# Performance work log

Measured on AMD Instinct MI355X. Metric: run time of the kernel, lower is better.

## Reference

```python
import jax, jax.numpy as jnp
import numpy as np

B, N, P, T = 128, 64, 128, 168


def setup_inputs() -> dict:
    key = jax.random.key(0)
    k1, k2, k3, k4, k5 = jax.random.split(key, 5)
    x = jax.random.normal(k1, (B, N, P), dtype=jnp.float32)
    x_i = jax.random.randint(k2, (B, P), 0, T)
    g = jax.random.normal(k3, (N * N, N * N), dtype=jnp.float32)
    weights = jax.random.normal(k4, (N * N, 1), dtype=jnp.float32)
    alphas = jax.random.uniform(k5, (1, T), dtype=jnp.float32)
    return {"x": x, "x_i": x_i, "g": g, "weights": weights, "alphas": alphas}


def reference(x, x_i, g, weights, alphas):
    # x: [b, N, p], x_i: [b, p] int in [0, T), g: [N*N, N*N]
    n = x.shape[1]
    F = (g @ (weights ** 2)) @ alphas          # [N*N, T]
    wg = F.T.reshape(-1, n, n)                 # [T, N, N]
    f_ = wg[x_i]                               # [b, p, N, N] (gather)
    xt = jnp.swapaxes(x, 1, 2)                 # [b, p, N]
    # matmul(f_, x_[...,None]) then sum over (p, last) == einsum then sum over p
    Z = jnp.einsum('bpij,bpj->bi', f_, xt)     # [b, N]
    return (Z, F)
```

## Files before the change

### kernel.cpp

```cpp
#include <hip/hip_runtime.h>
#include <hip/hip_bf16.h>


#define GN 4096
#define TT 168
#define BB 128
#define NN 64
#define PP 128

__global__ __launch_bounds__(256) void k_rowdot(
    const float* __restrict__ g, const float* __restrict__ w,
    const float* __restrict__ alphas, float* __restrict__ v,
    float* __restrict__ Fout) {
  const int row = blockIdx.x;
  const int t = threadIdx.x;
  const float4* g4 = (const float4*)(g + (size_t)row * GN);
  const float4* w4 = (const float4*)w;
  float s = 0.f;
#pragma unroll
  for (int it = 0; it < 4; ++it) {
    int idx = t + it * 256;
    float4 a = g4[idx];
    float4 b = w4[idx];
    s += a.x * (b.x * b.x) + a.y * (b.y * b.y) + a.z * (b.z * b.z) + a.w * (b.w * b.w);
  }
#pragma unroll
  for (int off = 32; off > 0; off >>= 1) s += __shfl_down(s, off, 64);
  __shared__ float ls[4];
  __shared__ float vsh;
  const int wave = t >> 6, lane = t & 63;
  if (lane == 0) ls[wave] = s;
  __syncthreads();
  if (t == 0) {
    float vi = ls[0] + ls[1] + ls[2] + ls[3];
    v[row] = vi;
    vsh = vi;
  }
  __syncthreads();
  const float vi = vsh;
  if (t < TT) Fout[(size_t)row * TT + t] = vi * alphas[t];
}

__global__ __launch_bounds__(256) void k_z(
    const float* __restrict__ x, const int* __restrict__ xi,
    const float* __restrict__ alphas, const float* __restrict__ v,
    float* __restrict__ Z) {
  const int b = blockIdx.x;
  const int t = threadIdx.x;
  __shared__ float ap[PP];
  __shared__ float y[NN];
  if (t < PP) ap[t] = alphas[xi[b * PP + t]];
  __syncthreads();
  const int j = t >> 2, r = t & 3;
  const float* xrow = x + (size_t)b * (NN * PP) + (size_t)j * PP;
  float s = 0.f;
#pragma unroll
  for (int k = 0; k < 32; ++k) {
    int p = r + 4 * k;
    s += ap[p] * xrow[p];
  }
  s += __shfl_down(s, 2, 64);
  s += __shfl_down(s, 1, 64);
  if (r == 0) y[j] = s;
  __syncthreads();
  if (t < NN) {
    const float* vrow = v + t * NN;
    float z = 0.f;
#pragma unroll
    for (int jj = 0; jj < NN; ++jj) z += vrow[jj] * y[jj];
    Z[b * NN + t] = z;
  }
}

extern "C" void kernel_launch(void* const* d_in, const int* in_sizes, int n_in,
                              void* d_out, int out_size, void* d_ws, size_t ws_size,
                              hipStream_t stream) {
  const float* x      = (const float*)d_in[0];
  const int*   xi     = (const int*)  d_in[1];
  const float* g      = (const float*)d_in[2];
  const float* w      = (const float*)d_in[3];
  const float* alphas = (const float*)d_in[4];

  float* Z    = (float*)d_out;
  float* Fout = (float*)d_out + (BB * NN);
  float* v    = (float*)d_ws;

  k_rowdot<<<GN, 256, 0, stream>>>(g, w, alphas, v, Fout);
  k_z<<<BB, 256, 0, stream>>>(x, xi, alphas, v, Z);
}
```

Baseline: 102.8 us.

## Fuse x-alpha reduction into g row-dot kernel, one wave per row

The first kernel now also computes the per-batch alpha-weighted reduction of x into a workspace buffer y, using extra blocks placed ahead of the g row-dot blocks. Each g row is now reduced by a single wave with nontemporal loads and xor shuffles, which removes the shared-memory cross-wave reduction and both barriers. The second kernel shrinks to a small v·y matvec with float4 loads. This aims to overlap the x work with the dominant 64MB g stream and shorten the serial tail, at the cost of fewer, longer-running blocks for the g pass.

```diff
diff --git a/kernel.cpp b/kernel.cpp
--- a/kernel.cpp
+++ b/kernel.cpp
@@ -1,5 +1,4 @@
 #include <hip/hip_runtime.h>
-#include <hip/hip_bf16.h>
 
 
 #define GN 4096
@@ -8,68 +7,71 @@
 #define NN 64
 #define PP 128
 
-__global__ __launch_bounds__(256) void k_rowdot(
+typedef float vf4 __attribute__((ext_vector_type(4)));
+
+__global__ __launch_bounds__(256) void k_fused(
+    const float* __restrict__ x, const int* __restrict__ xi,
     const float* __restrict__ g, const float* __restrict__ w,
     const float* __restrict__ alphas, float* __restrict__ v,
-    float* __restrict__ Fout) {
-  const int row = blockIdx.x;
+    float* __restrict__ y, float* __restrict__ Fout) {
   const int t = threadIdx.x;
-  const float4* g4 = (const float4*)(g + (size_t)row * GN);
-  const float4* w4 = (const float4*)w;
-  float s = 0.f;
+  if (blockIdx.x >= BB) {
+    const int rb = blockIdx.x - BB;
+    const int wave = t >> 6, lane = t & 63;
+    const int row = rb * 4 + wave;
+    const vf4* g4 = (const vf4*)(g + (size_t)row * GN);
+    const vf4* w4 = (const vf4*)w;
+    float s = 0.f;
+#pragma unroll 8
+    for (int it = 0; it < 16; ++it) {
+      vf4 a = __builtin_nontemporal_load(&g4[it * 64 + lane]);
+      vf4 b = w4[it * 64 + lane];
+      s += a.x * (b.x * b.x) + a.y * (b.y * b.y) +
+           a.z * (b.z * b.z) + a.w * (b.w * b.w);
+    }
 #pragma unroll
-  for (int it = 0; it < 4; ++it) {
-    int idx = t + it * 256;
-    float4 a = g4[idx];
-    float4 b = w4[idx];
-    s += a.x * (b.x * b.x) + a.y * (b.y * b.y) + a.z * (b.z * b.z) + a.w * (b.w * b.w);
+    for (int off = 32; off; off >>= 1) s += __shfl_xor(s, off, 64);
+    if (lane == 0) v[row] = s;
+    float* Frow = Fout + (size_t)row * TT;
+    Frow[lane]      = s * alphas[lane];
+    Frow[64 + lane] = s * alphas[64 + lane];
+    if (lane < TT - 128) Frow[128 + lane] = s * alphas[128 + lane];
+  } else {
+    const int b = blockIdx.x;
+    __shared__ float ap[PP];
+    if (t < PP) ap[t] = alphas[xi[b * PP + t]];
+    __syncthreads();
+    const int j = t >> 2, r = t & 3;
+    const float4* xrow4 =
+        (const float4*)(x + (size_t)b * (NN * PP) + (size_t)j * PP + r * 32);
+    const float4* ap4 = (const float4*)(ap + r * 32);
+    float s = 0.f;
+#pragma unroll
+    for (int k = 0; k < 8; ++k) {
+      float4 a = xrow4[k];
+      float4 c = ap4[k];
+      s += a.x * c.x + a.y * c.y + a.z * c.z + a.w * c.w;
+    }
+    s += __shfl_down(s, 2, 64);
+    s += __shfl_down(s, 1, 64);
+    if (r == 0) y[b * NN + j] = s;
   }
-#pragma unroll
-  for (int off = 32; off > 0; off >>= 1) s += __shfl_down(s, off, 64);
-  __shared__ float ls[4];
-  __shared__ float vsh;
-  const int wave = t >> 6, lane = t & 63;
-  if (lane == 0) ls[wave] = s;
-  __syncthreads();
-  if (t == 0) {
-    float vi = ls[0] + ls[1] + ls[2] + ls[3];
-    v[row] = vi;
-    vsh = vi;
-  }
-  __syncthreads();
-  const float vi = vsh;
-  if (t < TT) Fout[(size_t)row * TT + t] = vi * alphas[t];
 }
 
-__global__ __launch_bounds__(256) void k_z(
-    const float* __restrict__ x, const int* __restrict__ xi,
-    const float* __restrict__ alphas, const float* __restrict__ v,
+__global__ __launch_bounds__(64) void k_z2(
+    const float* __restrict__ v, const float* __restrict__ y,
     float* __restrict__ Z) {
-  const int b = blockIdx.x;
-  const int t = threadIdx.x;
-  __shared__ float ap[PP];
-  __shared__ float y[NN];
-  if (t < PP) ap[t] = alphas[xi[b * PP + t]];
-  __syncthreads();
-  const int j = t >> 2, r = t & 3;
-  const float* xrow = x + (size_t)b * (NN * PP) + (size_t)j * PP;
-  float s = 0.f;
+  const int b = blockIdx.x, i = threadIdx.x;
+  const float4* v4 = (const float4*)(v + i * NN);
+  const float4* y4 = (const float4*)(y + b * NN);
+  float z = 0.f;
 #pragma unroll
-  for (int k = 0; k < 32; ++k) {
-    int p = r + 4 * k;
-    s += ap[p] * xrow[p];
+  for (int q = 0; q < 16; ++q) {
+    float4 a = v4[q];
+    float4 c = y4[q];
+    z += a.x * c.x + a.y * c.y + a.z * c.z + a.w * c.w;
   }
-  s += __shfl_down(s, 2, 64);
-  s += __shfl_down(s, 1, 64);
-  if (r == 0) y[j] = s;
-  __syncthreads();
-  if (t < NN) {
-    const float* vrow = v + t * NN;
-    float z = 0.f;
-#pragma unroll
-    for (int jj = 0; jj < NN; ++jj) z += vrow[jj] * y[jj];
-    Z[b * NN + t] = z;
-  }
+  Z[b * NN + i] = z;
 }
 
 extern "C" void kernel_launch(void* const* d_in, const int* in_sizes, int n_in,
@@ -84,7 +86,8 @@
   float* Z    = (float*)d_out;
   float* Fout = (float*)d_out + (BB * NN);
   float* v    = (float*)d_ws;
+  float* y    = (float*)d_ws + GN;
 
-  k_rowdot<<<GN, 256, 0, stream>>>(g, w, alphas, v, Fout);
-  k_z<<<BB, 256, 0, stream>>>(x, xi, alphas, v, Z);
+  k_fused<<<BB + GN / 4, 256, 0, stream>>>(x, xi, g, w, alphas, v, y, Fout);
+  k_z2<<<BB, 64, 0, stream>>>(v, y, Z);
 }
```

Measured after the change: 111.7 us. 8.6% more time.
